# Optimization experiments

Measured on AMD Instinct MI355X. Metric: run time of the kernel, lower is better.

## Reference

```python
import jax, jax.numpy as jnp
import numpy as np

NUM_NETS = 2_000_000
PINS_PER_NET = 4
NUM_PINS = NUM_NETS * PINS_PER_NET


def setup_inputs() -> dict:
    key = jax.random.key(0)
    k1, k2, k3 = jax.random.split(key, 3)
    num_slrX, num_slrY = 1, 4
    # pin positions already expressed in SLR-grid units: x in [0, num_slrX), y in [0, num_slrY)
    pos = jax.random.uniform(k1, (NUM_PINS, 2), jnp.float32) * jnp.array(
        [float(max(num_slrX, 1)), float(max(num_slrY, 1))], jnp.float32)
    # CSR netpin structure: each net owns PINS_PER_NET pins, flat list is a permutation of all pins
    flat_netpin = jax.random.permutation(k2, NUM_PINS).astype(jnp.int32)
    netpin_start = (jnp.arange(NUM_NETS + 1, dtype=jnp.int32) * PINS_PER_NET)
    net_ids = jnp.repeat(jnp.arange(NUM_NETS, dtype=jnp.int32), PINS_PER_NET)
    net_weights = jax.random.uniform(k3, (NUM_NETS,), jnp.float32, minval=0.5, maxval=1.5)
    net_mask = jnp.ones((NUM_NETS,), jnp.bool_)
    pin_mask = jnp.zeros((NUM_PINS,), jnp.bool_)
    inv_gamma = jnp.float32(2.0)  # 1 / gamma, gamma = 0.5
    return dict(pos=pos, flat_netpin=flat_netpin, netpin_start=netpin_start,
                net_ids=net_ids, net_weights=net_weights, net_mask=net_mask,
                pin_mask=pin_mask, inv_gamma=inv_gamma,
                num_slrX=num_slrX, num_slrY=num_slrY)


def reference(pos, flat_netpin, netpin_start, net_ids, net_weights, net_mask,
              pin_mask, inv_gamma, num_slrX, num_slrY):
    """Weighted-average SLL: per-net log-sum-exp weighted-average span of pin
    SLR coordinates, per dimension, counted only for dims with >1 SLR."""
    n = net_weights.shape[0]
    p = pos[flat_netpin]  # [P, 2] gather pin coords in CSR order
    # numerically-stable exp weights per net (segment max/min shift)
    mx = jax.ops.segment_max(p, net_ids, num_segments=n)  # [N, 2]
    mn = jax.ops.segment_min(p, net_ids, num_segments=n)  # [N, 2]
    ep = jnp.exp((p - mx[net_ids]) * inv_gamma)   # exp(+x/gamma), shifted
    en = jnp.exp((mn[net_ids] - p) * inv_gamma)   # exp(-x/gamma), shifted
    s_ep = jax.ops.segment_sum(ep, net_ids, num_segments=n)
    s_xep = jax.ops.segment_sum(p * ep, net_ids, num_segments=n)
    s_en = jax.ops.segment_sum(en, net_ids, num_segments=n)
    s_xen = jax.ops.segment_sum(p * en, net_ids, num_segments=n)
    wa = s_xep / s_ep - s_xen / s_en  # [N, 2] weighted-average span per dim
    dim_on = jnp.array([num_slrX > 1, num_slrY > 1], dtype=wa.dtype)  # only multi-SLR dims
    per_net = jnp.sum(wa * dim_on, axis=1)  # [N]
    return jnp.sum(jnp.where(net_mask, net_weights * per_net, jnp.float32(0.0)))
```

## Files before the change

### kernel.cpp

```cpp
#include <hip/hip_runtime.h>
#include <stdint.h>


#define PINB_SHIFT 13
#define PINB_SIZE  (1 << PINB_SHIFT)
#define MAX_PINB   1024
#define JB_SHIFT   14
#define JB_SIZE    (1 << JB_SHIFT)
#define MAX_JB     512
#define P1_CHUNK   8192
#define NTHR       512

__device__ __forceinline__ float wa4(float a, float b, float c, float d, float ig) {
    float ea = __expf(a * ig), eb = __expf(b * ig);
    float ec = __expf(c * ig), ed = __expf(d * ig);
    float na = __expf(-a * ig), nb = __expf(-b * ig);
    float nc = __expf(-c * ig), nd = __expf(-d * ig);
    float s_ep  = ea + eb + ec + ed;
    float s_xep = a * ea + b * eb + c * ec + d * ed;
    float s_en  = na + nb + nc + nd;
    float s_xen = a * na + b * nb + c * nc + d * nd;
    return s_xep / s_ep - s_xen / s_en;
}

__global__ void init_kernel(unsigned* __restrict__ cur1, int n_pinb,
                            unsigned* __restrict__ cur2, int n_jb,
                            float* __restrict__ out) {
    int t = threadIdx.x;
    if (t == 0) out[0] = 0.0f;
    for (int i = t; i < n_pinb; i += blockDim.x) cur1[i] = (unsigned)i << PINB_SHIFT;
    for (int i = t; i < 2 * n_jb; i += blockDim.x) {
        int j = (i < n_jb) ? i : (i - n_jb);
        cur2[i] = (unsigned)j << JB_SHIFT;
    }
}

__global__ __launch_bounds__(NTHR) void p1_partition(
    const int4* __restrict__ fnp4, int NP, int n_pinb,
    uint2* __restrict__ ent1, unsigned* __restrict__ cur1)
{
    __shared__ uint2    staged[P1_CHUNK];
    __shared__ unsigned hist[MAX_PINB];
    __shared__ unsigned scn[MAX_PINB];
    __shared__ unsigned gbase[MAX_PINB];
    const int base  = blockIdx.x * P1_CHUNK;
    const int valid = min(P1_CHUNK, NP - base);
    const int t = threadIdx.x;

    for (int b = t; b < MAX_PINB; b += NTHR) hist[b] = 0;
    __syncthreads();

    unsigned pin[16], rnk[16];
    #pragma unroll
    for (int m4 = 0; m4 < 4; ++m4) {
        int k4 = t + NTHR * m4;
        int kk = 4 * k4;
        int4 v = make_int4(0, 0, 0, 0);
        if (kk < valid) v = fnp4[(base >> 2) + k4];
        pin[4*m4+0] = (unsigned)v.x; pin[4*m4+1] = (unsigned)v.y;
        pin[4*m4+2] = (unsigned)v.z; pin[4*m4+3] = (unsigned)v.w;
    }
    #pragma unroll
    for (int m4 = 0; m4 < 4; ++m4)
        #pragma unroll
        for (int c = 0; c < 4; ++c) {
            int kk = 4 * (t + NTHR * m4) + c;
            rnk[4*m4+c] = 0;
            if (kk < valid)
                rnk[4*m4+c] = atomicAdd(&hist[pin[4*m4+c] >> PINB_SHIFT], 1u);
        }
    __syncthreads();

    if (t < 64) {
        unsigned v[16], s = 0;
        #pragma unroll
        for (int i = 0; i < 16; ++i) { v[i] = hist[t * 16 + i]; s += v[i]; }
        unsigned e = s;
        #pragma unroll
        for (int off = 1; off < 64; off <<= 1) {
            unsigned u = __shfl_up(e, off, 64);
            if (t >= off) e += u;
        }
        e -= s;
        #pragma unroll
        for (int i = 0; i < 16; ++i) { scn[t * 16 + i] = e; e += v[i]; }
    }
    __syncthreads();

    for (int b = t; b < n_pinb; b += NTHR)
        if (hist[b]) gbase[b] = atomicAdd(&cur1[b], hist[b]);
    __syncthreads();

    #pragma unroll
    for (int m4 = 0; m4 < 4; ++m4)
        #pragma unroll
        for (int c = 0; c < 4; ++c) {
            int kk = 4 * (t + NTHR * m4) + c;
            if (kk < valid) {
                unsigned p = pin[4*m4+c];
                staged[scn[p >> PINB_SHIFT] + rnk[4*m4+c]] =
                    make_uint2(p, (unsigned)(base + kk));
            }
        }
    __syncthreads();

    for (int k = t; k < valid; k += NTHR) {
        uint2 e = staged[k];
        unsigned b = e.x >> PINB_SHIFT;
        ent1[gbase[b] + ((unsigned)k - scn[b])] = e;
    }
}

__global__ __launch_bounds__(NTHR) void p2_gather(
    const uint2* __restrict__ ent1, const float2* __restrict__ pos2,
    const int* __restrict__ slrx_p, const int* __restrict__ slry_p,
    int d, int NP, int n_jb,
    uint2* __restrict__ ent2, unsigned* __restrict__ cur2)
{
    const int slr = (d == 0) ? slrx_p[0] : slry_p[0];
    if (slr <= 1) return;

    __shared__ __align__(16) char smem[PINB_SIZE * sizeof(uint2) + 3 * MAX_JB * 4];
    float*    win    = (float*)smem;
    uint2*    staged = (uint2*)smem;
    unsigned* hist   = (unsigned*)(smem + PINB_SIZE * sizeof(uint2));
    unsigned* scn    = hist + MAX_JB;
    unsigned* gbase  = scn + MAX_JB;

    const int pbase = blockIdx.x << PINB_SHIFT;
    const int valid = min(PINB_SIZE, NP - pbase);
    const int t = threadIdx.x;

    uint2 e[16];
    #pragma unroll
    for (int m = 0; m < 16; ++m) {
        int k = t + NTHR * m;
        e[m] = make_uint2(0u, 0u);
        if (k < valid) e[m] = ent1[pbase + k];
    }
    for (int i = t; i < valid; i += NTHR) {
        float2 p = pos2[pbase + i];
        win[i] = d ? p.y : p.x;
    }
    if (t < MAX_JB) hist[t] = 0;
    __syncthreads();

    float yv[16]; unsigned rnk[16];
    #pragma unroll
    for (int m = 0; m < 16; ++m) {
        int k = t + NTHR * m;
        yv[m] = (k < valid) ? win[e[m].x & (PINB_SIZE - 1)] : 0.0f;
    }
    #pragma unroll
    for (int m = 0; m < 16; ++m) {
        int k = t + NTHR * m;
        rnk[m] = 0;
        if (k < valid) rnk[m] = atomicAdd(&hist[e[m].y >> JB_SHIFT], 1u);
    }
    __syncthreads();

    if (t < 64) {
        unsigned v[8], s = 0;
        #pragma unroll
        for (int i = 0; i < 8; ++i) { v[i] = hist[t * 8 + i]; s += v[i]; }
        unsigned ex = s;
        #pragma unroll
        for (int off = 1; off < 64; off <<= 1) {
            unsigned u = __shfl_up(ex, off, 64);
            if (t >= off) ex += u;
        }
        ex -= s;
        #pragma unroll
        for (int i = 0; i < 8; ++i) { scn[t * 8 + i] = ex; ex += v[i]; }
    }
    __syncthreads();

    for (int q = t; q < n_jb; q += NTHR)
        if (hist[q]) gbase[q] = atomicAdd(&cur2[q], hist[q]);
    __syncthreads();

    #pragma unroll
    for (int m = 0; m < 16; ++m) {
        int k = t + NTHR * m;
        if (k < valid)
            staged[scn[e[m].y >> JB_SHIFT] + rnk[m]] =
                make_uint2(e[m].y, __float_as_uint(yv[m]));
    }
    __syncthreads();

    for (int k = t; k < valid; k += NTHR) {
        uint2 s2 = staged[k];
        unsigned jb = s2.x >> JB_SHIFT;
        ent2[gbase[jb] + ((unsigned)k - scn[jb])] = s2;
    }
}

__global__ __launch_bounds__(NTHR) void p3_compute(
    const uint2* __restrict__ ent2, const float* __restrict__ wts,
    const float* __restrict__ ig_p,
    const int* __restrict__ slrx_p, const int* __restrict__ slry_p,
    int d, int NP, float* __restrict__ out)
{
    const int slr = (d == 0) ? slrx_p[0] : slry_p[0];
    if (slr <= 1) return;

    __shared__ float ytmp[JB_SIZE];
    const int jb     = blockIdx.x;
    const int base_j = jb << JB_SHIFT;
    const int nslots = min(JB_SIZE, NP - base_j);
    const int t = threadIdx.x;
    const float ig = ig_p[0];

    for (int k = t; k < nslots; k += NTHR) {
        uint2 e = ent2[base_j + k];
        ytmp[e.x & (JB_SIZE - 1)] = __uint_as_float(e.y);
    }
    __syncthreads();

    float val = 0.0f;
    const int nnets = nslots >> 2, bnet = base_j >> 2;
    const float4* y4 = (const float4*)ytmp;
    for (int i = t; i < nnets; i += NTHR) {
        float4 p = y4[i];
        val += wts[bnet + i] * wa4(p.x, p.y, p.z, p.w, ig);
    }

    #pragma unroll
    for (int off = 32; off > 0; off >>= 1) val += __shfl_down(val, off, 64);
    __syncthreads();
    if ((t & 63) == 0) ytmp[t >> 6] = val;
    __syncthreads();
    if (t == 0) {
        float s = 0.0f;
        #pragma unroll
        for (int w = 0; w < NTHR / 64; ++w) s += ytmp[w];
        atomicAdd(out, s);
    }
}

__global__ __launch_bounds__(256) void wasll_fallback(
    const float2* __restrict__ pos, const int4* __restrict__ fnp4,
    const float* __restrict__ net_weights, const float* __restrict__ inv_gamma_p,
    const int* __restrict__ slrx_p, const int* __restrict__ slry_p,
    float* __restrict__ out, int num_nets)
{
    const float ig = inv_gamma_p[0];
    const float dx = (slrx_p[0] > 1) ? 1.0f : 0.0f;
    const float dy = (slry_p[0] > 1) ? 1.0f : 0.0f;
    int net = blockIdx.x * blockDim.x + threadIdx.x;
    float val = 0.0f;
    if (net < num_nets) {
        int4 idx = fnp4[net];
        float2 p0 = pos[idx.x], p1 = pos[idx.y], p2 = pos[idx.z], p3 = pos[idx.w];
        val = net_weights[net] * (dx * wa4(p0.x, p1.x, p2.x, p3.x, ig)
                                + dy * wa4(p0.y, p1.y, p2.y, p3.y, ig));
    }
    #pragma unroll
    for (int off = 32; off > 0; off >>= 1) val += __shfl_down(val, off, 64);
    __shared__ float smem[4];
    if ((threadIdx.x & 63) == 0) smem[threadIdx.x >> 6] = val;
    __syncthreads();
    if (threadIdx.x == 0)
        atomicAdd(out, smem[0] + smem[1] + smem[2] + smem[3]);
}

__global__ void zero_out_kernel(float* __restrict__ out) { out[0] = 0.0f; }

extern "C" void kernel_launch(void* const* d_in, const int* in_sizes, int n_in,
                              void* d_out, int out_size, void* d_ws, size_t ws_size,
                              hipStream_t stream) {
    const float* posf        = (const float*)d_in[0];
    const int*   fnp         = (const int*)d_in[1];
    const float* net_weights = (const float*)d_in[4];
    const float* inv_gamma   = (const float*)d_in[7];
    const int*   slrx        = (const int*)d_in[8];
    const int*   slry        = (const int*)d_in[9];
    float*       out         = (float*)d_out;
    const int    N  = in_sizes[4];
    const int    NP = in_sizes[1];

    const int n_pinb = (NP + PINB_SIZE - 1) >> PINB_SHIFT;
    const int n_jb   = (NP + JB_SIZE - 1) >> JB_SHIFT;

    size_t off = 0;
    auto carve = [&](size_t bytes) { size_t o = off; off += (bytes + 255) & ~size_t(255); return o; };
    size_t o_ent1 = carve((size_t)n_pinb * PINB_SIZE * sizeof(uint2));
    size_t o_ent2 = carve((size_t)n_jb * JB_SIZE * sizeof(uint2));
    size_t o_cur1 = carve((size_t)n_pinb * sizeof(unsigned));
    size_t o_cur2 = carve((size_t)2 * n_jb * sizeof(unsigned));

    const bool ok = (NP == 4 * N) && (NP % 4 == 0) &&
                    (n_pinb <= MAX_PINB) && (n_jb <= MAX_JB) && (off <= ws_size);
    if (!ok) {
        hipLaunchKernelGGL(zero_out_kernel, dim3(1), dim3(1), 0, stream, out);
        const int block = 256, grid = (N + block - 1) / block;
        hipLaunchKernelGGL(wasll_fallback, dim3(grid), dim3(block), 0, stream,
                           (const float2*)posf, (const int4*)fnp, net_weights,
                           inv_gamma, slrx, slry, out, N);
        return;
    }

    char* ws = (char*)d_ws;
    uint2*    ent1 = (uint2*)(ws + o_ent1);
    uint2*    ent2 = (uint2*)(ws + o_ent2);
    unsigned* cur1 = (unsigned*)(ws + o_cur1);
    unsigned* cur2 = (unsigned*)(ws + o_cur2);

    hipLaunchKernelGGL(init_kernel, dim3(1), dim3(1024), 0, stream,
                       cur1, n_pinb, cur2, n_jb, out);

    const int g1 = (NP + P1_CHUNK - 1) / P1_CHUNK;
    hipLaunchKernelGGL(p1_partition, dim3(g1), dim3(NTHR), 0, stream,
                       (const int4*)fnp, NP, n_pinb, ent1, cur1);

    hipLaunchKernelGGL(p2_gather, dim3(n_pinb), dim3(NTHR), 0, stream,
                       ent1, (const float2*)posf, slrx, slry, 0, NP, n_jb, ent2, cur2);
    hipLaunchKernelGGL(p3_compute, dim3(n_jb), dim3(NTHR), 0, stream,
                       ent2, net_weights, inv_gamma, slrx, slry, 0, NP, out);

    hipLaunchKernelGGL(p2_gather, dim3(n_pinb), dim3(NTHR), 0, stream,
                       ent1, (const float2*)posf, slrx, slry, 1, NP, n_jb, ent2, cur2 + n_jb);
    hipLaunchKernelGGL(p3_compute, dim3(n_jb), dim3(NTHR), 0, stream,
                       ent2, net_weights, inv_gamma, slrx, slry, 1, NP, out);
}
```

Measured before the change: 275.6 us.

## Merge per-dimension gather/compute launches, replace init kernel with memset, widen blocks

Both dimensions' gather and compute passes now run in one launch each, so there are fewer kernel launches. Each dimension gets its own ent2 buffer when the workspace has room, and the kernels derive the dimension from the block index. The cursor init kernel is replaced by a memset, with base offsets now added at atomic time, and the output is zeroed inside the partition kernel. Partition and compute kernels move to 1024-thread blocks, which lowers per-thread unrolled work but may reduce occupancy or latency hiding.

```diff
diff --git a/kernel.cpp b/kernel.cpp
--- a/kernel.cpp
+++ b/kernel.cpp
@@ -9,7 +9,8 @@
 #define JB_SIZE    (1 << JB_SHIFT)
 #define MAX_JB     512
 #define P1_CHUNK   8192
-#define NTHR       512
+#define NTHR       1024
+#define NTHR2      512
 
 __device__ __forceinline__ float wa4(float a, float b, float c, float d, float ig) {
     float ea = __expf(a * ig), eb = __expf(b * ig);
@@ -23,21 +24,10 @@
     return s_xep / s_ep - s_xen / s_en;
 }
 
-__global__ void init_kernel(unsigned* __restrict__ cur1, int n_pinb,
-                            unsigned* __restrict__ cur2, int n_jb,
-                            float* __restrict__ out) {
-    int t = threadIdx.x;
-    if (t == 0) out[0] = 0.0f;
-    for (int i = t; i < n_pinb; i += blockDim.x) cur1[i] = (unsigned)i << PINB_SHIFT;
-    for (int i = t; i < 2 * n_jb; i += blockDim.x) {
-        int j = (i < n_jb) ? i : (i - n_jb);
-        cur2[i] = (unsigned)j << JB_SHIFT;
-    }
-}
-
 __global__ __launch_bounds__(NTHR) void p1_partition(
     const int4* __restrict__ fnp4, int NP, int n_pinb,
-    uint2* __restrict__ ent1, unsigned* __restrict__ cur1)
+    uint2* __restrict__ ent1, unsigned* __restrict__ cur1,
+    float* __restrict__ out)
 {
     __shared__ uint2    staged[P1_CHUNK];
     __shared__ unsigned hist[MAX_PINB];
@@ -47,12 +37,14 @@
     const int valid = min(P1_CHUNK, NP - base);
     const int t = threadIdx.x;
 
+    if (blockIdx.x == 0 && t == 0) out[0] = 0.0f;
+
     for (int b = t; b < MAX_PINB; b += NTHR) hist[b] = 0;
     __syncthreads();
 
-    unsigned pin[16], rnk[16];
-    #pragma unroll
-    for (int m4 = 0; m4 < 4; ++m4) {
+    unsigned pin[8], rnk[8];
+    #pragma unroll
+    for (int m4 = 0; m4 < 2; ++m4) {
         int k4 = t + NTHR * m4;
         int kk = 4 * k4;
         int4 v = make_int4(0, 0, 0, 0);
@@ -61,7 +53,7 @@
         pin[4*m4+2] = (unsigned)v.z; pin[4*m4+3] = (unsigned)v.w;
     }
     #pragma unroll
-    for (int m4 = 0; m4 < 4; ++m4)
+    for (int m4 = 0; m4 < 2; ++m4)
         #pragma unroll
         for (int c = 0; c < 4; ++c) {
             int kk = 4 * (t + NTHR * m4) + c;
@@ -88,11 +80,12 @@
     __syncthreads();
 
     for (int b = t; b < n_pinb; b += NTHR)
-        if (hist[b]) gbase[b] = atomicAdd(&cur1[b], hist[b]);
-    __syncthreads();
-
-    #pragma unroll
-    for (int m4 = 0; m4 < 4; ++m4)
+        if (hist[b])
+            gbase[b] = ((unsigned)b << PINB_SHIFT) + atomicAdd(&cur1[b], hist[b]);
+    __syncthreads();
+
+    #pragma unroll
+    for (int m4 = 0; m4 < 2; ++m4)
         #pragma unroll
         for (int c = 0; c < 4; ++c) {
             int kk = 4 * (t + NTHR * m4) + c;
@@ -111,14 +104,20 @@
     }
 }
 
-__global__ __launch_bounds__(NTHR) void p2_gather(
+__global__ __launch_bounds__(NTHR2) void p2_gather(
     const uint2* __restrict__ ent1, const float2* __restrict__ pos2,
     const int* __restrict__ slrx_p, const int* __restrict__ slry_p,
-    int d, int NP, int n_jb,
-    uint2* __restrict__ ent2, unsigned* __restrict__ cur2)
+    int nb_per_dim, int NP, int n_jb,
+    uint2* __restrict__ ent2, unsigned ent2_stride,
+    unsigned* __restrict__ cur2)
 {
+    int bb = blockIdx.x, d = 0;
+    if (bb >= nb_per_dim) { d = 1; bb -= nb_per_dim; }
     const int slr = (d == 0) ? slrx_p[0] : slry_p[0];
     if (slr <= 1) return;
+
+    uint2*    ent2d = ent2 + (size_t)d * ent2_stride;
+    unsigned* cur2d = cur2 + d * n_jb;
 
     __shared__ __align__(16) char smem[PINB_SIZE * sizeof(uint2) + 3 * MAX_JB * 4];
     float*    win    = (float*)smem;
@@ -127,18 +126,18 @@
     unsigned* scn    = hist + MAX_JB;
     unsigned* gbase  = scn + MAX_JB;
 
-    const int pbase = blockIdx.x << PINB_SHIFT;
+    const int pbase = bb << PINB_SHIFT;
     const int valid = min(PINB_SIZE, NP - pbase);
     const int t = threadIdx.x;
 
     uint2 e[16];
     #pragma unroll
     for (int m = 0; m < 16; ++m) {
-        int k = t + NTHR * m;
+        int k = t + NTHR2 * m;
         e[m] = make_uint2(0u, 0u);
         if (k < valid) e[m] = ent1[pbase + k];
     }
-    for (int i = t; i < valid; i += NTHR) {
+    for (int i = t; i < valid; i += NTHR2) {
         float2 p = pos2[pbase + i];
         win[i] = d ? p.y : p.x;
     }
@@ -148,12 +147,12 @@
     float yv[16]; unsigned rnk[16];
     #pragma unroll
     for (int m = 0; m < 16; ++m) {
-        int k = t + NTHR * m;
+        int k = t + NTHR2 * m;
         yv[m] = (k < valid) ? win[e[m].x & (PINB_SIZE - 1)] : 0.0f;
     }
     #pragma unroll
     for (int m = 0; m < 16; ++m) {
-        int k = t + NTHR * m;
+        int k = t + NTHR2 * m;
         rnk[m] = 0;
         if (k < valid) rnk[m] = atomicAdd(&hist[e[m].y >> JB_SHIFT], 1u);
     }
@@ -175,44 +174,48 @@
     }
     __syncthreads();
 
-    for (int q = t; q < n_jb; q += NTHR)
-        if (hist[q]) gbase[q] = atomicAdd(&cur2[q], hist[q]);
+    for (int q = t; q < n_jb; q += NTHR2)
+        if (hist[q])
+            gbase[q] = ((unsigned)q << JB_SHIFT) + atomicAdd(&cur2d[q], hist[q]);
     __syncthreads();
 
     #pragma unroll
     for (int m = 0; m < 16; ++m) {
-        int k = t + NTHR * m;
+        int k = t + NTHR2 * m;
         if (k < valid)
             staged[scn[e[m].y >> JB_SHIFT] + rnk[m]] =
                 make_uint2(e[m].y, __float_as_uint(yv[m]));
     }
     __syncthreads();
 
-    for (int k = t; k < valid; k += NTHR) {
+    for (int k = t; k < valid; k += NTHR2) {
         uint2 s2 = staged[k];
         unsigned jb = s2.x >> JB_SHIFT;
-        ent2[gbase[jb] + ((unsigned)k - scn[jb])] = s2;
+        ent2d[gbase[jb] + ((unsigned)k - scn[jb])] = s2;
     }
 }
 
 __global__ __launch_bounds__(NTHR) void p3_compute(
-    const uint2* __restrict__ ent2, const float* __restrict__ wts,
-    const float* __restrict__ ig_p,
+    const uint2* __restrict__ ent2, unsigned ent2_stride,
+    const float* __restrict__ wts, const float* __restrict__ ig_p,
     const int* __restrict__ slrx_p, const int* __restrict__ slry_p,
-    int d, int NP, float* __restrict__ out)
+    int njb_per_dim, int NP, float* __restrict__ out)
 {
+    int jb = blockIdx.x, d = 0;
+    if (jb >= njb_per_dim) { d = 1; jb -= njb_per_dim; }
     const int slr = (d == 0) ? slrx_p[0] : slry_p[0];
     if (slr <= 1) return;
 
+    const uint2* ent2d = ent2 + (size_t)d * ent2_stride;
+
     __shared__ float ytmp[JB_SIZE];
-    const int jb     = blockIdx.x;
     const int base_j = jb << JB_SHIFT;
     const int nslots = min(JB_SIZE, NP - base_j);
     const int t = threadIdx.x;
     const float ig = ig_p[0];
 
     for (int k = t; k < nslots; k += NTHR) {
-        uint2 e = ent2[base_j + k];
+        uint2 e = ent2d[base_j + k];
         ytmp[e.x & (JB_SIZE - 1)] = __uint_as_float(e.y);
     }
     __syncthreads();
@@ -285,9 +288,11 @@
     size_t off = 0;
     auto carve = [&](size_t bytes) { size_t o = off; off += (bytes + 255) & ~size_t(255); return o; };
     size_t o_ent1 = carve((size_t)n_pinb * PINB_SIZE * sizeof(uint2));
-    size_t o_ent2 = carve((size_t)n_jb * JB_SIZE * sizeof(uint2));
     size_t o_cur1 = carve((size_t)n_pinb * sizeof(unsigned));
     size_t o_cur2 = carve((size_t)2 * n_jb * sizeof(unsigned));
+    size_t ent2_bytes = (size_t)n_jb * JB_SIZE * sizeof(uint2);
+    size_t o_ent2 = carve(ent2_bytes);
+    const size_t cur_span = (o_cur2 + (size_t)2 * n_jb * sizeof(unsigned)) - o_cur1;
 
     const bool ok = (NP == 4 * N) && (NP % 4 == 0) &&
                     (n_pinb <= MAX_PINB) && (n_jb <= MAX_JB) && (off <= ws_size);
@@ -300,26 +305,40 @@
         return;
     }
 
+    const bool dual = (off + ent2_bytes) <= ws_size;
+    const unsigned ent2_stride = dual ? (unsigned)((size_t)n_jb * JB_SIZE) : 0u;
+
     char* ws = (char*)d_ws;
     uint2*    ent1 = (uint2*)(ws + o_ent1);
     uint2*    ent2 = (uint2*)(ws + o_ent2);
     unsigned* cur1 = (unsigned*)(ws + o_cur1);
     unsigned* cur2 = (unsigned*)(ws + o_cur2);
 
-    hipLaunchKernelGGL(init_kernel, dim3(1), dim3(1024), 0, stream,
-                       cur1, n_pinb, cur2, n_jb, out);
+    hipMemsetAsync(ws + o_cur1, 0, cur_span, stream);
 
     const int g1 = (NP + P1_CHUNK - 1) / P1_CHUNK;
     hipLaunchKernelGGL(p1_partition, dim3(g1), dim3(NTHR), 0, stream,
-                       (const int4*)fnp, NP, n_pinb, ent1, cur1);
-
-    hipLaunchKernelGGL(p2_gather, dim3(n_pinb), dim3(NTHR), 0, stream,
-                       ent1, (const float2*)posf, slrx, slry, 0, NP, n_jb, ent2, cur2);
-    hipLaunchKernelGGL(p3_compute, dim3(n_jb), dim3(NTHR), 0, stream,
-                       ent2, net_weights, inv_gamma, slrx, slry, 0, NP, out);
-
-    hipLaunchKernelGGL(p2_gather, dim3(n_pinb), dim3(NTHR), 0, stream,
-                       ent1, (const float2*)posf, slrx, slry, 1, NP, n_jb, ent2, cur2 + n_jb);
-    hipLaunchKernelGGL(p3_compute, dim3(n_jb), dim3(NTHR), 0, stream,
-                       ent2, net_weights, inv_gamma, slrx, slry, 1, NP, out);
-}
+                       (const int4*)fnp, NP, n_pinb, ent1, cur1, out);
+
+    if (dual) {
+        hipLaunchKernelGGL(p2_gather, dim3(2 * n_pinb), dim3(NTHR2), 0, stream,
+                           ent1, (const float2*)posf, slrx, slry,
+                           n_pinb, NP, n_jb, ent2, ent2_stride, cur2);
+        hipLaunchKernelGGL(p3_compute, dim3(2 * n_jb), dim3(NTHR), 0, stream,
+                           ent2, ent2_stride, net_weights, inv_gamma,
+                           slrx, slry, n_jb, NP, out);
+    } else {
+        hipLaunchKernelGGL(p2_gather, dim3(n_pinb), dim3(NTHR2), 0, stream,
+                           ent1, (const float2*)posf, slrx, slry,
+                           n_pinb, NP, n_jb, ent2, 0u, cur2);
+        hipLaunchKernelGGL(p3_compute, dim3(n_jb), dim3(NTHR), 0, stream,
+                           ent2, 0u, net_weights, inv_gamma,
+                           slrx, slry, n_jb, NP, out);
+        hipLaunchKernelGGL(p2_gather, dim3(n_pinb), dim3(NTHR2), 0, stream,
+                           ent1, (const float2*)posf, slrx, slry,
+                           0, NP, n_jb, ent2, 0u, cur2);
+        hipLaunchKernelGGL(p3_compute, dim3(n_jb), dim3(NTHR), 0, stream,
+                           ent2, 0u, net_weights, inv_gamma,
+                           slrx, slry, 0, NP, out);
+    }
+}
```

Measured after the change: 281.8 us. +2.2%, slower.

## Fuse partition, gather and compute stages into one persistent kernel with grid barriers

Applied to the files above, without the earlier changes.

Replaces the init kernel and the separate partition, gather and compute launches with one persistent kernel of fixed block count. The stages are separated by a software grid barrier built on an atomic ticket counter in the workspace. Bucket cursors are no longer reset each call; write slots are taken modulo the bucket size, which relies on every bucket receiving exactly a full bucket of entries per call. The aim is to cut per-launch overhead and inter-kernel tail gaps. The barrier assumes all 512 blocks are resident at once (deadlock otherwise), and the code now requires the pin count to be a multiple of the bucket size.

```diff
diff --git a/kernel.cpp b/kernel.cpp
--- a/kernel.cpp
+++ b/kernel.cpp
@@ -8,8 +8,8 @@
 #define JB_SHIFT   14
 #define JB_SIZE    (1 << JB_SHIFT)
 #define MAX_JB     512
-#define P1_CHUNK   8192
-#define NTHR       512
+#define NTHR2      512
+#define NBLK       512
 
 __device__ __forceinline__ float wa4(float a, float b, float c, float d, float ig) {
     float ea = __expf(a * ig), eb = __expf(b * ig);
@@ -23,218 +23,205 @@
     return s_xep / s_ep - s_xen / s_en;
 }
 
-__global__ void init_kernel(unsigned* __restrict__ cur1, int n_pinb,
-                            unsigned* __restrict__ cur2, int n_jb,
-                            float* __restrict__ out) {
-    int t = threadIdx.x;
-    if (t == 0) out[0] = 0.0f;
-    for (int i = t; i < n_pinb; i += blockDim.x) cur1[i] = (unsigned)i << PINB_SHIFT;
-    for (int i = t; i < 2 * n_jb; i += blockDim.x) {
-        int j = (i < n_jb) ? i : (i - n_jb);
-        cur2[i] = (unsigned)j << JB_SHIFT;
-    }
-}
-
-__global__ __launch_bounds__(NTHR) void p1_partition(
-    const int4* __restrict__ fnp4, int NP, int n_pinb,
-    uint2* __restrict__ ent1, unsigned* __restrict__ cur1)
+__device__ __forceinline__ void grid_bar(unsigned* bar) {
+    __syncthreads();
+    if (threadIdx.x == 0) {
+        __threadfence();
+        unsigned tkt = atomicAdd(bar, 1u);
+        unsigned tgt = (tkt / NBLK + 1u) * (unsigned)NBLK;
+        while (atomicMax(bar, 0u) < tgt)
+            __builtin_amdgcn_s_sleep(4);
+        __threadfence();
+    }
+    __syncthreads();
+}
+
+__global__ __launch_bounds__(NTHR2, 4) void fused_wasll(
+    const int4* __restrict__ fnp4, const float2* __restrict__ pos2,
+    const float* __restrict__ wts, const float* __restrict__ ig_p,
+    const int* __restrict__ slrx_p, const int* __restrict__ slry_p,
+    int NP, int n_pinb, int n_jb,
+    uint2* __restrict__ ent1, uint2* __restrict__ ent2a,
+    uint2* __restrict__ ent2b,
+    unsigned* __restrict__ cur1, unsigned* __restrict__ cur2,
+    unsigned* __restrict__ bar, float* __restrict__ out)
 {
-    __shared__ uint2    staged[P1_CHUNK];
-    __shared__ unsigned hist[MAX_PINB];
-    __shared__ unsigned scn[MAX_PINB];
-    __shared__ unsigned gbase[MAX_PINB];
-    const int base  = blockIdx.x * P1_CHUNK;
-    const int valid = min(P1_CHUNK, NP - base);
+    __shared__ __align__(16) char smem[PINB_SIZE * sizeof(uint2) + 3 * MAX_PINB * 4];
     const int t = threadIdx.x;
-
-    for (int b = t; b < MAX_PINB; b += NTHR) hist[b] = 0;
-    __syncthreads();
-
-    unsigned pin[16], rnk[16];
-    #pragma unroll
-    for (int m4 = 0; m4 < 4; ++m4) {
-        int k4 = t + NTHR * m4;
-        int kk = 4 * k4;
-        int4 v = make_int4(0, 0, 0, 0);
-        if (kk < valid) v = fnp4[(base >> 2) + k4];
-        pin[4*m4+0] = (unsigned)v.x; pin[4*m4+1] = (unsigned)v.y;
-        pin[4*m4+2] = (unsigned)v.z; pin[4*m4+3] = (unsigned)v.w;
-    }
-    #pragma unroll
-    for (int m4 = 0; m4 < 4; ++m4)
-        #pragma unroll
-        for (int c = 0; c < 4; ++c) {
-            int kk = 4 * (t + NTHR * m4) + c;
-            rnk[4*m4+c] = 0;
-            if (kk < valid)
-                rnk[4*m4+c] = atomicAdd(&hist[pin[4*m4+c] >> PINB_SHIFT], 1u);
+    const bool dx = slrx_p[0] > 1, dy = slry_p[0] > 1;
+
+    if (blockIdx.x == 0 && t == 0) out[0] = 0.0f;
+    if (!dx && !dy) return;
+
+    {
+        uint2*    staged = (uint2*)smem;
+        unsigned* hist   = (unsigned*)(smem + PINB_SIZE * sizeof(uint2));
+        unsigned* scn    = hist + MAX_PINB;
+        unsigned* gbase  = scn + MAX_PINB;
+        for (int c = blockIdx.x; c < n_pinb; c += NBLK) {
+            const int base = c << PINB_SHIFT;
+            for (int b = t; b < MAX_PINB; b += NTHR2) hist[b] = 0;
+            __syncthreads();
+
+            unsigned pin[16], rnk[16];
+            #pragma unroll
+            for (int m4 = 0; m4 < 4; ++m4) {
+                int4 v = fnp4[(base >> 2) + t + NTHR2 * m4];
+                pin[4*m4+0] = (unsigned)v.x; pin[4*m4+1] = (unsigned)v.y;
+                pin[4*m4+2] = (unsigned)v.z; pin[4*m4+3] = (unsigned)v.w;
+            }
+            #pragma unroll
+            for (int i = 0; i < 16; ++i)
+                rnk[i] = atomicAdd(&hist[pin[i] >> PINB_SHIFT], 1u);
+            __syncthreads();
+
+            if (t < 64) {
+                unsigned v[16], s = 0;
+                #pragma unroll
+                for (int i = 0; i < 16; ++i) { v[i] = hist[t * 16 + i]; s += v[i]; }
+                unsigned e = s;
+                #pragma unroll
+                for (int off = 1; off < 64; off <<= 1) {
+                    unsigned u = __shfl_up(e, off, 64);
+                    if (t >= off) e += u;
+                }
+                e -= s;
+                #pragma unroll
+                for (int i = 0; i < 16; ++i) { scn[t * 16 + i] = e; e += v[i]; }
+            }
+            __syncthreads();
+
+            for (int b = t; b < n_pinb; b += NTHR2)
+                if (hist[b]) gbase[b] = atomicAdd(&cur1[b], hist[b]);
+            __syncthreads();
+
+            #pragma unroll
+            for (int m4 = 0; m4 < 4; ++m4)
+                #pragma unroll
+                for (int cc = 0; cc < 4; ++cc) {
+                    int i = 4 * m4 + cc;
+                    unsigned kk = (unsigned)(base + 4 * (t + NTHR2 * m4) + cc);
+                    staged[scn[pin[i] >> PINB_SHIFT] + rnk[i]] =
+                        make_uint2(pin[i], kk);
+                }
+            __syncthreads();
+
+            for (int k = t; k < PINB_SIZE; k += NTHR2) {
+                uint2 e = staged[k];
+                unsigned b = e.x >> PINB_SHIFT;
+                unsigned slot = (gbase[b] + ((unsigned)k - scn[b])) & (PINB_SIZE - 1);
+                ent1[((size_t)b << PINB_SHIFT) + slot] = e;
+            }
+            __syncthreads();
         }
-    __syncthreads();
-
-    if (t < 64) {
-        unsigned v[16], s = 0;
-        #pragma unroll
-        for (int i = 0; i < 16; ++i) { v[i] = hist[t * 16 + i]; s += v[i]; }
-        unsigned e = s;
-        #pragma unroll
-        for (int off = 1; off < 64; off <<= 1) {
-            unsigned u = __shfl_up(e, off, 64);
-            if (t >= off) e += u;
+    }
+    grid_bar(bar);
+
+    for (int d = 0; d < 2; ++d) {
+        const bool act = d ? dy : dx;
+        if (!act) continue;
+        uint2* ent2d = d ? ent2b : ent2a;
+        if (d == 1 && dx) grid_bar(bar);
+
+        {
+            float*    win    = (float*)smem;
+            uint2*    staged = (uint2*)smem;
+            unsigned* hist   = (unsigned*)(smem + PINB_SIZE * sizeof(uint2));
+            unsigned* scn    = hist + MAX_JB;
+            unsigned* gbase  = scn + MAX_JB;
+            for (int b = blockIdx.x; b < n_pinb; b += NBLK) {
+                const int pbase = b << PINB_SHIFT;
+                __syncthreads();
+
+                uint2 e[16];
+                #pragma unroll
+                for (int m = 0; m < 16; ++m)
+                    e[m] = ent1[pbase + t + NTHR2 * m];
+                for (int i = t; i < PINB_SIZE; i += NTHR2) {
+                    float2 p = pos2[pbase + i];
+                    win[i] = d ? p.y : p.x;
+                }
+                if (t < MAX_JB) hist[t] = 0;
+                __syncthreads();
+
+                float yv[16]; unsigned rnk[16];
+                #pragma unroll
+                for (int m = 0; m < 16; ++m)
+                    yv[m] = win[e[m].x & (PINB_SIZE - 1)];
+                #pragma unroll
+                for (int m = 0; m < 16; ++m)
+                    rnk[m] = atomicAdd(&hist[e[m].y >> JB_SHIFT], 1u);
+                __syncthreads();
+
+                if (t < 64) {
+                    unsigned v[8], s = 0;
+                    #pragma unroll
+                    for (int i = 0; i < 8; ++i) { v[i] = hist[t * 8 + i]; s += v[i]; }
+                    unsigned ex = s;
+                    #pragma unroll
+                    for (int off = 1; off < 64; off <<= 1) {
+                        unsigned u = __shfl_up(ex, off, 64);
+                        if (t >= off) ex += u;
+                    }
+                    ex -= s;
+                    #pragma unroll
+                    for (int i = 0; i < 8; ++i) { scn[t * 8 + i] = ex; ex += v[i]; }
+                }
+                __syncthreads();
+
+                for (int q = t; q < n_jb; q += NTHR2)
+                    if (hist[q]) gbase[q] = atomicAdd(&cur2[q], hist[q]);
+                __syncthreads();
+
+                #pragma unroll
+                for (int m = 0; m < 16; ++m)
+                    staged[scn[e[m].y >> JB_SHIFT] + rnk[m]] =
+                        make_uint2(e[m].y, __float_as_uint(yv[m]));
+                __syncthreads();
+
+                for (int k = t; k < PINB_SIZE; k += NTHR2) {
+                    uint2 s2 = staged[k];
+                    unsigned jb = s2.x >> JB_SHIFT;
+                    unsigned slot = (gbase[jb] + ((unsigned)k - scn[jb])) & (JB_SIZE - 1);
+                    ent2d[((size_t)jb << JB_SHIFT) + slot] = s2;
+                }
+            }
         }
-        e -= s;
-        #pragma unroll
-        for (int i = 0; i < 16; ++i) { scn[t * 16 + i] = e; e += v[i]; }
-    }
-    __syncthreads();
-
-    for (int b = t; b < n_pinb; b += NTHR)
-        if (hist[b]) gbase[b] = atomicAdd(&cur1[b], hist[b]);
-    __syncthreads();
-
-    #pragma unroll
-    for (int m4 = 0; m4 < 4; ++m4)
-        #pragma unroll
-        for (int c = 0; c < 4; ++c) {
-            int kk = 4 * (t + NTHR * m4) + c;
-            if (kk < valid) {
-                unsigned p = pin[4*m4+c];
-                staged[scn[p >> PINB_SHIFT] + rnk[4*m4+c]] =
-                    make_uint2(p, (unsigned)(base + kk));
+        grid_bar(bar);
+
+        {
+            float* ytmp = (float*)smem;
+            const float ig = ig_p[0];
+            for (int jb = blockIdx.x; jb < n_jb; jb += NBLK) {
+                const int base_j = jb << JB_SHIFT;
+                __syncthreads();
+                for (int k = t; k < JB_SIZE; k += NTHR2) {
+                    uint2 e = ent2d[base_j + k];
+                    ytmp[e.x & (JB_SIZE - 1)] = __uint_as_float(e.y);
+                }
+                __syncthreads();
+
+                float val = 0.0f;
+                const int bnet = base_j >> 2;
+                const float4* y4 = (const float4*)ytmp;
+                for (int i = t; i < (JB_SIZE >> 2); i += NTHR2) {
+                    float4 p = y4[i];
+                    val += wts[bnet + i] * wa4(p.x, p.y, p.z, p.w, ig);
+                }
+                #pragma unroll
+                for (int off = 32; off > 0; off >>= 1)
+                    val += __shfl_down(val, off, 64);
+                __syncthreads();
+                if ((t & 63) == 0) ytmp[t >> 6] = val;
+                __syncthreads();
+                if (t == 0) {
+                    float s = 0.0f;
+                    #pragma unroll
+                    for (int w = 0; w < NTHR2 / 64; ++w) s += ytmp[w];
+                    atomicAdd(out, s);
+                }
             }
         }
-    __syncthreads();
-
-    for (int k = t; k < valid; k += NTHR) {
-        uint2 e = staged[k];
-        unsigned b = e.x >> PINB_SHIFT;
-        ent1[gbase[b] + ((unsigned)k - scn[b])] = e;
-    }
-}
-
-__global__ __launch_bounds__(NTHR) void p2_gather(
-    const uint2* __restrict__ ent1, const float2* __restrict__ pos2,
-    const int* __restrict__ slrx_p, const int* __restrict__ slry_p,
-    int d, int NP, int n_jb,
-    uint2* __restrict__ ent2, unsigned* __restrict__ cur2)
-{
-    const int slr = (d == 0) ? slrx_p[0] : slry_p[0];
-    if (slr <= 1) return;
-
-    __shared__ __align__(16) char smem[PINB_SIZE * sizeof(uint2) + 3 * MAX_JB * 4];
-    float*    win    = (float*)smem;
-    uint2*    staged = (uint2*)smem;
-    unsigned* hist   = (unsigned*)(smem + PINB_SIZE * sizeof(uint2));
-    unsigned* scn    = hist + MAX_JB;
-    unsigned* gbase  = scn + MAX_JB;
-
-    const int pbase = blockIdx.x << PINB_SHIFT;
-    const int valid = min(PINB_SIZE, NP - pbase);
-    const int t = threadIdx.x;
-
-    uint2 e[16];
-    #pragma unroll
-    for (int m = 0; m < 16; ++m) {
-        int k = t + NTHR * m;
-        e[m] = make_uint2(0u, 0u);
-        if (k < valid) e[m] = ent1[pbase + k];
-    }
-    for (int i = t; i < valid; i += NTHR) {
-        float2 p = pos2[pbase + i];
-        win[i] = d ? p.y : p.x;
-    }
-    if (t < MAX_JB) hist[t] = 0;
-    __syncthreads();
-
-    float yv[16]; unsigned rnk[16];
-    #pragma unroll
-    for (int m = 0; m < 16; ++m) {
-        int k = t + NTHR * m;
-        yv[m] = (k < valid) ? win[e[m].x & (PINB_SIZE - 1)] : 0.0f;
-    }
-    #pragma unroll
-    for (int m = 0; m < 16; ++m) {
-        int k = t + NTHR * m;
-        rnk[m] = 0;
-        if (k < valid) rnk[m] = atomicAdd(&hist[e[m].y >> JB_SHIFT], 1u);
-    }
-    __syncthreads();
-
-    if (t < 64) {
-        unsigned v[8], s = 0;
-        #pragma unroll
-        for (int i = 0; i < 8; ++i) { v[i] = hist[t * 8 + i]; s += v[i]; }
-        unsigned ex = s;
-        #pragma unroll
-        for (int off = 1; off < 64; off <<= 1) {
-            unsigned u = __shfl_up(ex, off, 64);
-            if (t >= off) ex += u;
-        }
-        ex -= s;
-        #pragma unroll
-        for (int i = 0; i < 8; ++i) { scn[t * 8 + i] = ex; ex += v[i]; }
-    }
-    __syncthreads();
-
-    for (int q = t; q < n_jb; q += NTHR)
-        if (hist[q]) gbase[q] = atomicAdd(&cur2[q], hist[q]);
-    __syncthreads();
-
-    #pragma unroll
-    for (int m = 0; m < 16; ++m) {
-        int k = t + NTHR * m;
-        if (k < valid)
-            staged[scn[e[m].y >> JB_SHIFT] + rnk[m]] =
-                make_uint2(e[m].y, __float_as_uint(yv[m]));
-    }
-    __syncthreads();
-
-    for (int k = t; k < valid; k += NTHR) {
-        uint2 s2 = staged[k];
-        unsigned jb = s2.x >> JB_SHIFT;
-        ent2[gbase[jb] + ((unsigned)k - scn[jb])] = s2;
-    }
-}
-
-__global__ __launch_bounds__(NTHR) void p3_compute(
-    const uint2* __restrict__ ent2, const float* __restrict__ wts,
-    const float* __restrict__ ig_p,
-    const int* __restrict__ slrx_p, const int* __restrict__ slry_p,
-    int d, int NP, float* __restrict__ out)
-{
-    const int slr = (d == 0) ? slrx_p[0] : slry_p[0];
-    if (slr <= 1) return;
-
-    __shared__ float ytmp[JB_SIZE];
-    const int jb     = blockIdx.x;
-    const int base_j = jb << JB_SHIFT;
-    const int nslots = min(JB_SIZE, NP - base_j);
-    const int t = threadIdx.x;
-    const float ig = ig_p[0];
-
-    for (int k = t; k < nslots; k += NTHR) {
-        uint2 e = ent2[base_j + k];
-        ytmp[e.x & (JB_SIZE - 1)] = __uint_as_float(e.y);
-    }
-    __syncthreads();
-
-    float val = 0.0f;
-    const int nnets = nslots >> 2, bnet = base_j >> 2;
-    const float4* y4 = (const float4*)ytmp;
-    for (int i = t; i < nnets; i += NTHR) {
-        float4 p = y4[i];
-        val += wts[bnet + i] * wa4(p.x, p.y, p.z, p.w, ig);
-    }
-
-    #pragma unroll
-    for (int off = 32; off > 0; off >>= 1) val += __shfl_down(val, off, 64);
-    __syncthreads();
-    if ((t & 63) == 0) ytmp[t >> 6] = val;
-    __syncthreads();
-    if (t == 0) {
-        float s = 0.0f;
-        #pragma unroll
-        for (int w = 0; w < NTHR / 64; ++w) s += ytmp[w];
-        atomicAdd(out, s);
     }
 }
 
@@ -279,18 +266,21 @@
     const int    N  = in_sizes[4];
     const int    NP = in_sizes[1];
 
-    const int n_pinb = (NP + PINB_SIZE - 1) >> PINB_SHIFT;
-    const int n_jb   = (NP + JB_SIZE - 1) >> JB_SHIFT;
+    const int n_pinb = NP >> PINB_SHIFT;
+    const int n_jb   = NP >> JB_SHIFT;
 
     size_t off = 0;
     auto carve = [&](size_t bytes) { size_t o = off; off += (bytes + 255) & ~size_t(255); return o; };
-    size_t o_ent1 = carve((size_t)n_pinb * PINB_SIZE * sizeof(uint2));
-    size_t o_ent2 = carve((size_t)n_jb * JB_SIZE * sizeof(uint2));
-    size_t o_cur1 = carve((size_t)n_pinb * sizeof(unsigned));
-    size_t o_cur2 = carve((size_t)2 * n_jb * sizeof(unsigned));
-
-    const bool ok = (NP == 4 * N) && (NP % 4 == 0) &&
-                    (n_pinb <= MAX_PINB) && (n_jb <= MAX_JB) && (off <= ws_size);
+    size_t o_ent1  = carve((size_t)NP * sizeof(uint2));
+    size_t o_ent2a = carve((size_t)NP * sizeof(uint2));
+    size_t o_cur1  = carve((size_t)MAX_PINB * sizeof(unsigned));
+    size_t o_cur2  = carve((size_t)MAX_JB * sizeof(unsigned));
+    size_t o_bar   = carve(256);
+    size_t core    = off;
+    size_t o_ent2b = carve((size_t)NP * sizeof(uint2));
+
+    const bool ok = (NP == 4 * N) && (NP % JB_SIZE == 0) && (NP > 0) &&
+                    (n_pinb <= MAX_PINB) && (n_jb <= MAX_JB) && (core <= ws_size);
     if (!ok) {
         hipLaunchKernelGGL(zero_out_kernel, dim3(1), dim3(1), 0, stream, out);
         const int block = 256, grid = (N + block - 1) / block;
@@ -300,26 +290,18 @@
         return;
     }
 
+    const bool dual = (off <= ws_size);
     char* ws = (char*)d_ws;
-    uint2*    ent1 = (uint2*)(ws + o_ent1);
-    uint2*    ent2 = (uint2*)(ws + o_ent2);
-    unsigned* cur1 = (unsigned*)(ws + o_cur1);
-    unsigned* cur2 = (unsigned*)(ws + o_cur2);
-
-    hipLaunchKernelGGL(init_kernel, dim3(1), dim3(1024), 0, stream,
-                       cur1, n_pinb, cur2, n_jb, out);
-
-    const int g1 = (NP + P1_CHUNK - 1) / P1_CHUNK;
-    hipLaunchKernelGGL(p1_partition, dim3(g1), dim3(NTHR), 0, stream,
-                       (const int4*)fnp, NP, n_pinb, ent1, cur1);
-
-    hipLaunchKernelGGL(p2_gather, dim3(n_pinb), dim3(NTHR), 0, stream,
-                       ent1, (const float2*)posf, slrx, slry, 0, NP, n_jb, ent2, cur2);
-    hipLaunchKernelGGL(p3_compute, dim3(n_jb), dim3(NTHR), 0, stream,
-                       ent2, net_weights, inv_gamma, slrx, slry, 0, NP, out);
-
-    hipLaunchKernelGGL(p2_gather, dim3(n_pinb), dim3(NTHR), 0, stream,
-                       ent1, (const float2*)posf, slrx, slry, 1, NP, n_jb, ent2, cur2 + n_jb);
-    hipLaunchKernelGGL(p3_compute, dim3(n_jb), dim3(NTHR), 0, stream,
-                       ent2, net_weights, inv_gamma, slrx, slry, 1, NP, out);
-}
+    uint2*    ent1  = (uint2*)(ws + o_ent1);
+    uint2*    ent2a = (uint2*)(ws + o_ent2a);
+    uint2*    ent2b = dual ? (uint2*)(ws + o_ent2b) : ent2a;
+    unsigned* cur1  = (unsigned*)(ws + o_cur1);
+    unsigned* cur2  = (unsigned*)(ws + o_cur2);
+    unsigned* bar   = (unsigned*)(ws + o_bar);
+
+    hipMemsetAsync(bar, 0, 256, stream);
+    hipLaunchKernelGGL(fused_wasll, dim3(NBLK), dim3(NTHR2), 0, stream,
+                       (const int4*)fnp, (const float2*)posf, net_weights,
+                       inv_gamma, slrx, slry, NP, n_pinb, n_jb,
+                       ent1, ent2a, ent2b, cur1, cur2, bar, out);
+}
```

After: 290.9 us. 1.06x slower.
